# Kernel optimization log

Hardware: AMD Instinct MI355X
Metric: run time of the kernel (lower is better)

## Reference

```python
import jax, jax.numpy as jnp
import numpy as np

B, N, D = 8, 64, 512          # batch, latent tokens, token dim
C, H, W, P = 256, 128, 128, 36  # img feat channels/HW, sampling points
PG = 128                       # parameter-generator inner dim (0.25*D)
HEADS = 8                      # D // 64
TOT = C * C + P * P            # adaptive mixing param count per token


def _ln(x, g, b):
    m = x.mean(-1, keepdims=True)
    v = x.var(-1, keepdims=True)
    return (x - m) / jnp.sqrt(v + 1e-5) * g + b


def _gelu(x):
    return jax.nn.gelu(x, approximate=False)


def _grid_sample(img, grid):
    # img: (B,C,H,W); grid: (B,N,P,2) in [-1,1]; bilinear, border pad, align_corners=False
    Bi, Ci, Hi, Wi = img.shape
    x = ((grid[..., 0] + 1.0) * Wi - 1.0) * 0.5
    y = ((grid[..., 1] + 1.0) * Hi - 1.0) * 0.5
    x0 = jnp.floor(x)
    y0 = jnp.floor(y)
    wx = x - x0
    wy = y - y0
    x0i = jnp.clip(x0.astype(jnp.int32), 0, Wi - 1)
    x1i = jnp.clip(x0.astype(jnp.int32) + 1, 0, Wi - 1)
    y0i = jnp.clip(y0.astype(jnp.int32), 0, Hi - 1)
    y1i = jnp.clip(y0.astype(jnp.int32) + 1, 0, Hi - 1)
    imgt = img.transpose(0, 2, 3, 1)  # (B,H,W,C)
    bidx = jnp.arange(Bi)[:, None, None]
    v00 = imgt[bidx, y0i, x0i]  # (B,N,P,C)
    v01 = imgt[bidx, y0i, x1i]
    v10 = imgt[bidx, y1i, x0i]
    v11 = imgt[bidx, y1i, x1i]
    wx = wx[..., None]
    wy = wy[..., None]
    return (v00 * (1 - wx) * (1 - wy) + v01 * wx * (1 - wy)
            + v10 * (1 - wx) * wy + v11 * wx * wy)


def setup_inputs() -> dict:
    key = jax.random.key(0)
    ks = jax.random.split(key, 16)
    rn = lambda k, s, sc: jax.random.normal(k, s, jnp.float32) * sc
    tl = jax.random.uniform(ks[0], (B, N, 2), jnp.float32) * 0.5
    wh = 0.2 + jax.random.uniform(ks[1], (B, N, 2), jnp.float32) * 0.4
    return dict(
        token_embed=rn(ks[2], (B, N, D), 1.0),
        token_roi=jnp.concatenate([tl, tl + wh], axis=-1),
        img_feat=rn(ks[3], (B, C, H, W), 1.0),
        ln_off_g=jnp.ones(D), ln_off_b=jnp.zeros(D),
        w_off=rn(ks[4], (D, P * 2), D ** -0.5),
        roi_offset_bias=rn(ks[5], (P * 2,), 1.0),
        ln_pg_g=jnp.ones(D), ln_pg_b=jnp.zeros(D),
        w_pg1=rn(ks[6], (D, PG), D ** -0.5), b_pg1=jnp.zeros(PG),
        w_pg2=rn(ks[7], (PG, TOT), 0.02 * PG ** -0.5),
        b_pg2=rn(ks[8], (TOT,), 0.02),
        m_beta=jnp.zeros(C), s_beta=jnp.zeros(P),
        w_out=rn(ks[9], (P * C, D), (P * C) ** -0.5), b_out=jnp.zeros(D),
        ln1_g=jnp.ones(D), ln1_b=jnp.zeros(D),
        w_qkv=rn(ks[10], (D, 3 * D), D ** -0.5), b_qkv=jnp.zeros(3 * D),
        w_proj=rn(ks[11], (D, D), D ** -0.5), b_proj=jnp.zeros(D),
        ln2_g=jnp.ones(D), ln2_b=jnp.zeros(D),
        w_fc1=rn(ks[12], (D, 4 * D), D ** -0.5), b_fc1=jnp.zeros(4 * D),
        w_fc2=rn(ks[13], (4 * D, D), (4 * D) ** -0.5), b_fc2=jnp.zeros(D),
    )


def reference(token_embed, token_roi, img_feat,
              ln_off_g, ln_off_b, w_off, roi_offset_bias,
              ln_pg_g, ln_pg_b, w_pg1, b_pg1, w_pg2, b_pg2,
              m_beta, s_beta, w_out, b_out,
              ln1_g, ln1_b, w_qkv, b_qkv, w_proj, b_proj,
              ln2_g, ln2_b, w_fc1, b_fc1, w_fc2, b_fc2):
    Bq, Nq, Dm = token_embed.shape
    # --- OP.SAMPLING_M: offsets -> absolute points (n_heads=1) ---
    off = _ln(token_embed, ln_off_g, ln_off_b) @ w_off + roi_offset_bias  # (B,N,2P)
    off = off.reshape(Bq, Nq, 1, P, 2)
    mu = off.mean(-2, keepdims=True)
    sd = jnp.std(off, axis=-2, keepdims=True, ddof=1) + 1e-5  # unbiased, as torch.std
    off = (off - mu) / (3.0 * sd)
    xy = (token_roi[..., 2:] + token_roi[..., :2]) * 0.5
    wh = token_roi[..., 2:] - token_roi[..., :2]
    pts = xy[:, :, None, None, :] + off * wh[:, :, None, None, :]  # (B,N,1,P,2)
    grid = pts.reshape(Bq, Nq, P, 2) * 2.0 - 1.0
    sampled = _grid_sample(img_feat, grid)  # (B,N,P,C)
    # --- adaptive mixing (AdaMixer): per-token generated channel/spatial weights ---
    q = _ln(token_embed, ln_pg_g, ln_pg_b)
    params = (q @ w_pg1 + b_pg1) @ w_pg2 + b_pg2  # (B,N,TOT)
    cm = params[..., :C * C].reshape(Bq, Nq, C, C)
    sm = params[..., C * C:].reshape(Bq, Nq, P, P)
    h = _gelu(jnp.einsum('bnpc,bncd->bnpd', sampled, cm) + m_beta)
    h = _gelu(jnp.einsum('bnqp,bnpd->bnqd', sm, h) + s_beta[:, None])
    token_embed = token_embed + (h.reshape(Bq, Nq, P * C) @ w_out + b_out)
    # --- OP.ATTN ---
    x = _ln(token_embed, ln1_g, ln1_b)
    hd = Dm // HEADS
    qkv = (x @ w_qkv + b_qkv).reshape(Bq, Nq, 3, HEADS, hd)
    qh, kh, vh = qkv[:, :, 0], qkv[:, :, 1], qkv[:, :, 2]
    att = jax.nn.softmax(jnp.einsum('bqhd,bkhd->bhqk', qh, kh) * hd ** -0.5, axis=-1)
    o = jnp.einsum('bhqk,bkhd->bqhd', att, vh).reshape(Bq, Nq, Dm)
    token_embed = token_embed + (o @ w_proj + b_proj)
    # --- OP.MLP ---
    x = _ln(token_embed, ln2_g, ln2_b)
    token_embed = token_embed + (_gelu(x @ w_fc1 + b_fc1) @ w_fc2 + b_fc2)
    return token_embed
```

## Files before the change

### kernel.cpp

```cpp
#include <hip/hip_runtime.h>
#include <hip/hip_bf16.h>

typedef __hip_bfloat16 bf16;
typedef __attribute__((ext_vector_type(8))) short short8;
typedef __attribute__((ext_vector_type(4))) short s16x4;
typedef __attribute__((ext_vector_type(4))) float f32x4;

#define NTOK 512
#define TOTC 66832
#define CM_SZ 65536

__device__ __forceinline__ float b2f(bf16 x) { return __bfloat162float(x); }
__device__ __forceinline__ bf16 f2b(float x) { return __float2bfloat16(x); }
__device__ __forceinline__ float gelu_f(float x) {
  return 0.5f * x * (1.0f + erff(x * 0.7071067811865476f));
}
__device__ __forceinline__ f32x4 mfma16(short8 a, short8 b, f32x4 c) {
  return __builtin_amdgcn_mfma_f32_16x16x32_bf16(a, b, c, 0, 0, 0);
}

__global__ __launch_bounds__(256) void k_head(
    const float* __restrict__ te, const float* __restrict__ roi,
    const float* __restrict__ g_off, const float* __restrict__ b_off,
    const float* __restrict__ w_off, const float* __restrict__ off_bias,
    const float* __restrict__ g_pg, const float* __restrict__ b_pg,
    const float* __restrict__ w_pg1, const float* __restrict__ b_pg1,
    bf16* __restrict__ t_out, int* __restrict__ meta_i, float* __restrict__ meta_w,
    const float* __restrict__ img, bf16* __restrict__ imgT,
    const float* __restrict__ w0, bf16* __restrict__ o0,
    const float* __restrict__ w1, bf16* __restrict__ o1,
    const float* __restrict__ w2, bf16* __restrict__ o2,
    const float* __restrict__ w3, bf16* __restrict__ o3,
    const float* __restrict__ w4, bf16* __restrict__ o4) {
  __shared__ __align__(16) char smem_raw[16896];
  int blk = blockIdx.x;
  int t = threadIdx.x;
  if (blk < 512) {
    int tok = blk;
    int lane = t & 63, w = t >> 6;
    float* xo = (float*)smem_raw;
    float* xq = xo + 512;
    float* offb = xq + 512;
    float* red = offb + 72;
    float* wsum = red + 4;
    size_t base = (size_t)tok * 512;
    float a0 = te[base + t];
    float a1 = te[base + t + 256];
    float s = a0 + a1;
#pragma unroll
    for (int o = 32; o; o >>= 1) s += __shfl_xor(s, o);
    if (lane == 0) wsum[w] = s;
    __syncthreads();
    float mean = (wsum[0] + wsum[1] + wsum[2] + wsum[3]) * (1.0f / 512.0f);
    float d0 = a0 - mean, d1 = a1 - mean;
    float ss = d0 * d0 + d1 * d1;
#pragma unroll
    for (int o = 32; o; o >>= 1) ss += __shfl_xor(ss, o);
    __syncthreads();
    if (lane == 0) wsum[w] = ss;
    __syncthreads();
    float var = (wsum[0] + wsum[1] + wsum[2] + wsum[3]) * (1.0f / 512.0f);
    float rstd = rsqrtf(var + 1e-5f);
    xo[t] = d0 * rstd * g_off[t] + b_off[t];
    xo[t + 256] = d1 * rstd * g_off[t + 256] + b_off[t + 256];
    xq[t] = d0 * rstd * g_pg[t] + b_pg[t];
    xq[t + 256] = d1 * rstd * g_pg[t + 256] + b_pg[t + 256];
    __syncthreads();
    if (t < 128) {
      float acc = b_pg1[t];
      for (int d = 0; d < 512; ++d) acc = fmaf(xq[d], w_pg1[d * 128 + t], acc);
      t_out[(size_t)tok * 128 + t] = f2b(acc);
    } else if (t < 200) {
      int j = t - 128;
      float acc = off_bias[j];
      for (int d = 0; d < 512; ++d) acc = fmaf(xo[d], w_off[d * 72 + j], acc);
      offb[j] = acc;
    }
    __syncthreads();
    if (t < 2) {
      float mu = 0.f;
      for (int p = 0; p < 36; ++p) mu += offb[p * 2 + t];
      mu *= (1.0f / 36.0f);
      float s2 = 0.f;
      for (int p = 0; p < 36; ++p) { float dd = offb[p * 2 + t] - mu; s2 += dd * dd; }
      float sd = sqrtf(s2 * (1.0f / 35.0f)) + 1e-5f;
      red[t] = mu;
      red[2 + t] = 1.0f / (3.0f * sd);
    }
    __syncthreads();
    if (t < 36) {
      int p = t;
      float r0 = roi[tok * 4 + 0], r1 = roi[tok * 4 + 1];
      float r2 = roi[tok * 4 + 2], r3 = roi[tok * 4 + 3];
      float cx = (r0 + r2) * 0.5f, cy = (r1 + r3) * 0.5f;
      float bw = r2 - r0, bh = r3 - r1;
      float ox = (offb[p * 2 + 0] - red[0]) * red[2];
      float oy = (offb[p * 2 + 1] - red[1]) * red[3];
      float fx = (cx + ox * bw) * 128.0f - 0.5f;
      float fy = (cy + oy * bh) * 128.0f - 0.5f;
      float x0f = floorf(fx), y0f = floorf(fy);
      float wx = fx - x0f, wy = fy - y0f;
      int x0 = min(max((int)x0f, 0), 127);
      int x1 = min(max((int)x0f + 1, 0), 127);
      int y0 = min(max((int)y0f, 0), 127);
      int y1 = min(max((int)y0f + 1, 0), 127);
      int ibase = (tok >> 6) * 16384;
      int mi = (tok * 36 + p) * 4;
      meta_i[mi + 0] = (ibase + y0 * 128 + x0) * 256;
      meta_i[mi + 1] = (ibase + y0 * 128 + x1) * 256;
      meta_i[mi + 2] = (ibase + y1 * 128 + x0) * 256;
      meta_i[mi + 3] = (ibase + y1 * 128 + x1) * 256;
      meta_w[mi + 0] = (1.f - wx) * (1.f - wy);
      meta_w[mi + 1] = wx * (1.f - wy);
      meta_w[mi + 2] = (1.f - wx) * wy;
      meta_w[mi + 3] = wx * wy;
    }
  } else if (blk < 4608) {
    int bb = blk - 512;
    int b = bb >> 9;
    int hw0 = (bb & 511) * 32;
    bf16 (*tile2)[264] = (bf16(*)[264])smem_raw;
    int hw = t & 31, c0 = t >> 5;
#pragma unroll 8
    for (int i = 0; i < 32; ++i) {
      int c = c0 + 8 * i;
      tile2[hw][c] = f2b(img[((size_t)(b * 256 + c) << 14) + hw0 + hw]);
    }
    __syncthreads();
    int c8 = (t & 31) * 8, hwl = t >> 5;
#pragma unroll
    for (int p = 0; p < 4; ++p) {
      int h2 = hwl + 8 * p;
      *(short8*)&imgT[(((size_t)b << 14) + hw0 + h2) * 256 + c8] =
          *(const short8*)&tile2[h2][c8];
    }
  } else {
    int b = blk - 4608;
    const float* W;
    bf16* O;
    int K, N, loc;
    if (b < 4608) { W = w0; O = o0; K = 9216; N = 512; loc = b; }
    else if (b < 5376) { W = w1; O = o1; K = 512; N = 1536; loc = b - 4608; }
    else if (b < 5632) { W = w2; O = o2; K = 512; N = 512; loc = b - 5376; }
    else if (b < 6656) { W = w3; O = o3; K = 512; N = 2048; loc = b - 5632; }
    else { W = w4; O = o4; K = 2048; N = 512; loc = b - 6656; }
    int ntn = N >> 5;
    int nb = loc % ntn, kb = loc / ntn;
    int n0 = nb * 32, k0 = kb * 32;
    float (*tl)[33] = (float(*)[33])smem_raw;
    int r = t >> 5, c = t & 31;
#pragma unroll
    for (int i = 0; i < 4; ++i)
      tl[r + 8 * i][c] = W[(size_t)(k0 + r + 8 * i) * N + n0 + c];
    __syncthreads();
    int n_l = t >> 3, k4 = (t & 7) * 4;
    bf16 tmp[4];
#pragma unroll
    for (int j = 0; j < 4; ++j) tmp[j] = f2b(tl[k4 + j][n_l]);
    *(s16x4*)&O[(size_t)(n0 + n_l) * K + k0 + k4] = *(const s16x4*)tmp;
  }
}

__global__ __launch_bounds__(256) void k_samp_pg2(
    const bf16* __restrict__ tb16, const float* __restrict__ w2,
    const float* __restrict__ b2, bf16* __restrict__ pchunk,
    const bf16* __restrict__ imgT, const int* __restrict__ meta_i,
    const float* __restrict__ meta_w, bf16* __restrict__ S) {
  __shared__ bf16 BsT[64][136];
  int blk = blockIdx.x;
  int t = threadIdx.x;
  if (blk < 2090) {
    int n0 = (blk % 1045) * 64;
    int row0 = (blk / 1045) * 256;
    int lane = t & 63, w = t >> 6;
    int quad = lane >> 4, l16 = lane & 15;
    {
      int nl = (t & 15) * 4, kk = t >> 4;
#pragma unroll
      for (int pass = 0; pass < 8; ++pass) {
        int k = kk + pass * 16;
        int n = n0 + nl;
        int nc = (n + 3 < TOTC) ? n : (TOTC - 4);
        const float4 v = *(const float4*)(w2 + (size_t)k * TOTC + nc);
        BsT[nl + 0][k] = f2b(v.x);
        BsT[nl + 1][k] = f2b(v.y);
        BsT[nl + 2][k] = f2b(v.z);
        BsT[nl + 3][k] = f2b(v.w);
      }
    }
    __syncthreads();
    f32x4 acc[4][4];
#pragma unroll
    for (int i = 0; i < 4; ++i)
#pragma unroll
      for (int j = 0; j < 4; ++j) acc[i][j] = (f32x4){0.f, 0.f, 0.f, 0.f};
    const bf16* Abase = tb16 + ((size_t)(row0 + w * 64 + l16)) * 128 + quad * 8;
#pragma unroll
    for (int ks = 0; ks < 4; ++ks) {
      short8 af[4], bff[4];
#pragma unroll
      for (int mt = 0; mt < 4; ++mt)
        af[mt] = *(const short8*)(Abase + mt * 16 * 128 + ks * 32);
#pragma unroll
      for (int nt = 0; nt < 4; ++nt)
        bff[nt] = *(const short8*)(&BsT[nt * 16 + l16][ks * 32 + quad * 8]);
#pragma unroll
      for (int mt = 0; mt < 4; ++mt)
#pragma unroll
        for (int nt = 0; nt < 4; ++nt)
          acc[mt][nt] = mfma16(af[mt], bff[nt], acc[mt][nt]);
    }
    float bias_r[4];
#pragma unroll
    for (int nt = 0; nt < 4; ++nt) {
      int col = n0 + nt * 16 + l16;
      bias_r[nt] = (col < TOTC) ? b2[col] : 0.f;
    }
    bf16* stg = &BsT[0][0];
#pragma unroll
    for (int mt = 0; mt < 4; ++mt) {
      __syncthreads();
#pragma unroll
      for (int nt = 0; nt < 4; ++nt)
#pragma unroll
        for (int r = 0; r < 4; ++r)
          stg[(w * 16 + quad * 4 + r) * 72 + nt * 16 + l16] =
              f2b(acc[mt][nt][r] + bias_r[nt]);
      __syncthreads();
#pragma unroll
      for (int pass = 0; pass < 2; ++pass) {
        int t2 = t + pass * 256;
        int row_l = t2 >> 3;
        int wi = row_l >> 4, rr = row_l & 15;
        int c8 = (t2 & 7) * 8;
        int col = n0 + c8;
        if (col < TOTC) {
          int grow = row0 + wi * 64 + mt * 16 + rr;
          *(short8*)&pchunk[(size_t)grow * TOTC + col] =
              *(const short8*)&stg[(wi * 16 + rr) * 72 + c8];
        }
      }
    }
  } else {
    int tok = blk - 2090;
#pragma unroll 6
    for (int p = 0; p < 36; ++p) {
      int mi = (tok * 36 + p) * 4;
      int o00 = meta_i[mi + 0], o01 = meta_i[mi + 1], o10 = meta_i[mi + 2], o11 = meta_i[mi + 3];
      float w00 = meta_w[mi + 0], w01 = meta_w[mi + 1], w10 = meta_w[mi + 2], w11 = meta_w[mi + 3];
      float v = w00 * b2f(imgT[o00 + t]) + w01 * b2f(imgT[o01 + t]) +
                w10 * b2f(imgT[o10 + t]) + w11 * b2f(imgT[o11 + t]);
      S[((size_t)tok * 36 + p) * 256 + t] = f2b(v);
    }
  }
}

__global__ __launch_bounds__(256) void k_mix3(const bf16* __restrict__ pchunk,
                                              const bf16* __restrict__ S,
                                              const float* __restrict__ m_beta,
                                              const float* __restrict__ s_beta,
                                              bf16* __restrict__ h2) {
  int tok = blockIdx.x, dh = blockIdx.y * 128;
  int t = threadIdx.x, lane = t & 63, w = t >> 6;
  int quad = lane >> 4, l16 = lane & 15;
  __shared__ bf16 h1T[128][72];
  __shared__ bf16 smS[48][72];
  __shared__ short cmw[4][32][40];
  for (int i = t; i < 1728; i += 256) ((unsigned*)smS)[i] = 0u;
  __syncthreads();
  const bf16* sm = pchunk + (size_t)tok * TOTC + CM_SZ;
  for (int i = t; i < 1296; i += 256) {
    int q = i / 36, p = i - q * 36;
    smS[q][p] = sm[i];
  }
  f32x4 acc[3][2];
#pragma unroll
  for (int i = 0; i < 3; ++i)
#pragma unroll
    for (int j = 0; j < 2; ++j) acc[i][j] = (f32x4){0.f, 0.f, 0.f, 0.f};
  const bf16* Sg = S + (size_t)tok * 9216;
  const bf16* Cg = pchunk + (size_t)tok * TOTC;
  int dw = w * 32;
  int c_l = lane & 31;
  int dtop = (lane >> 5) * 16;
  const bf16* src0 = Cg + (size_t)c_l * 256 + dh + dw + dtop;
  short8 v0 = *(const short8*)src0;
  short8 v1 = *(const short8*)(src0 + 8);
#pragma unroll
  for (int kc = 0; kc < 256; kc += 32) {
#pragma unroll
    for (int j = 0; j < 8; ++j) cmw[w][dtop + j][c_l] = v0[j];
#pragma unroll
    for (int j = 0; j < 8; ++j) cmw[w][dtop + 8 + j][c_l] = v1[j];
    short8 a[3];
#pragma unroll
    for (int mt = 0; mt < 3; ++mt)
      a[mt] = *(const short8*)(Sg + (size_t)(mt * 16 + l16) * 256 + kc + quad * 8);
    short8 v0n, v1n;
    if (kc < 224) {
      const bf16* srcn = Cg + (size_t)(kc + 32 + c_l) * 256 + dh + dw + dtop;
      v0n = *(const short8*)srcn;
      v1n = *(const short8*)(srcn + 8);
    }
    asm volatile("" ::: "memory");
    short8 bfr[2];
#pragma unroll
    for (int nt = 0; nt < 2; ++nt)
      bfr[nt] = *(const short8*)&cmw[w][nt * 16 + l16][quad * 8];
#pragma unroll
    for (int mt = 0; mt < 3; ++mt)
#pragma unroll
      for (int nt = 0; nt < 2; ++nt)
        acc[mt][nt] = mfma16(a[mt], bfr[nt], acc[mt][nt]);
    asm volatile("" ::: "memory");
    v0 = v0n;
    v1 = v1n;
  }
#pragma unroll
  for (int nt = 0; nt < 2; ++nt) {
    int dl = dw + nt * 16 + l16;
    float mb = m_beta[dh + dl];
#pragma unroll
    for (int mt = 0; mt < 3; ++mt)
#pragma unroll
      for (int r = 0; r < 4; ++r) {
        int p = mt * 16 + quad * 4 + r;
        if (p < 36) h1T[dl][p] = f2b(gelu_f(acc[mt][nt][r] + mb));
      }
  }
  for (int i = t; i < 128 * 28; i += 256) {
    int d = i / 28, p = 36 + i % 28;
    h1T[d][p] = (bf16)0.f;
  }
  __syncthreads();
  f32x4 acc2[3][2];
#pragma unroll
  for (int i = 0; i < 3; ++i)
#pragma unroll
    for (int j = 0; j < 2; ++j) acc2[i][j] = (f32x4){0.f, 0.f, 0.f, 0.f};
#pragma unroll
  for (int ks = 0; ks < 2; ++ks) {
    short8 a2[3], b2v[2];
#pragma unroll
    for (int mt = 0; mt < 3; ++mt)
      a2[mt] = *(const short8*)&smS[mt * 16 + l16][ks * 32 + quad * 8];
#pragma unroll
    for (int nt = 0; nt < 2; ++nt)
      b2v[nt] = *(const short8*)&h1T[dw + nt * 16 + l16][ks * 32 + quad * 8];
#pragma unroll
    for (int mt = 0; mt < 3; ++mt)
#pragma unroll
      for (int nt = 0; nt < 2; ++nt)
        acc2[mt][nt] = mfma16(a2[mt], b2v[nt], acc2[mt][nt]);
  }
  bf16* h2p = h2 + (size_t)tok * 9216 + dh;
#pragma unroll
  for (int mt = 0; mt < 3; ++mt)
#pragma unroll
    for (int r = 0; r < 4; ++r) {
      int q = mt * 16 + quad * 4 + r;
      if (q >= 36) continue;
      float sb = s_beta[q];
#pragma unroll
      for (int nt = 0; nt < 2; ++nt)
        h2p[q * 256 + dw + nt * 16 + l16] = f2b(gelu_f(acc2[mt][nt][r] + sb));
    }
}

__global__ __launch_bounds__(256) void k_gemm_bt(const bf16* __restrict__ A,
                                                 const bf16* __restrict__ BT,
                                                 float* __restrict__ part,
                                                 int M, int N, int K) {
  int nb = blockIdx.x, mb = blockIdx.y, ks = blockIdx.z;
  int kchunk = K / gridDim.z;
  int k0 = ks * kchunk;
  __shared__ bf16 As[64][72], Bs[64][72];
  int t = threadIdx.x, lane = t & 63, w = t >> 6;
  int quad = lane >> 4, l16 = lane & 15;
  int wm = (w >> 1) * 32, wn = (w & 1) * 32;
  int r = t >> 2, kk = (t & 3) * 16;
  f32x4 acc[2][2];
#pragma unroll
  for (int i = 0; i < 2; ++i)
#pragma unroll
    for (int j = 0; j < 2; ++j) acc[i][j] = (f32x4){0.f, 0.f, 0.f, 0.f};
  for (int kt = 0; kt < kchunk; kt += 64) {
    __syncthreads();
    const bf16* ga = A + (size_t)(mb * 64 + r) * K + k0 + kt + kk;
    *(short8*)&As[r][kk] = *(const short8*)ga;
    *(short8*)&As[r][kk + 8] = *(const short8*)(ga + 8);
    const bf16* gb = BT + (size_t)(nb * 64 + r) * K + k0 + kt + kk;
    *(short8*)&Bs[r][kk] = *(const short8*)gb;
    *(short8*)&Bs[r][kk + 8] = *(const short8*)(gb + 8);
    __syncthreads();
#pragma unroll
    for (int kss = 0; kss < 2; ++kss) {
      short8 af[2], bff[2];
#pragma unroll
      for (int mt = 0; mt < 2; ++mt)
        af[mt] = *(const short8*)&As[wm + mt * 16 + l16][kss * 32 + quad * 8];
#pragma unroll
      for (int nt = 0; nt < 2; ++nt)
        bff[nt] = *(const short8*)&Bs[wn + nt * 16 + l16][kss * 32 + quad * 8];
#pragma unroll
      for (int mt = 0; mt < 2; ++mt)
#pragma unroll
        for (int nt = 0; nt < 2; ++nt)
          acc[mt][nt] = mfma16(af[mt], bff[nt], acc[mt][nt]);
    }
  }
#pragma unroll
  for (int mt = 0; mt < 2; ++mt)
#pragma unroll
    for (int rr = 0; rr < 4; ++rr) {
      int m = mb * 64 + wm + mt * 16 + quad * 4 + rr;
#pragma unroll
      for (int nt = 0; nt < 2; ++nt) {
        int n = nb * 64 + wn + nt * 16 + l16;
        part[(size_t)ks * M * N + (size_t)m * N + n] = acc[mt][nt][rr];
      }
    }
}

__global__ __launch_bounds__(256) void k_gemm_ep(const bf16* __restrict__ A,
                                                 const bf16* __restrict__ BT,
                                                 const float* __restrict__ bias,
                                                 int M, int N, int K, int do_gelu,
                                                 float* __restrict__ outf,
                                                 bf16* __restrict__ outh) {
  int nb = blockIdx.x, mb = blockIdx.y;
  __shared__ bf16 As[64][72], Bs[64][72];
  int t = threadIdx.x, lane = t & 63, w = t >> 6;
  int quad = lane >> 4, l16 = lane & 15;
  int wm = (w >> 1) * 32, wn = (w & 1) * 32;
  int r = t >> 2, kk = (t & 3) * 16;
  f32x4 acc[2][2];
#pragma unroll
  for (int i = 0; i < 2; ++i)
#pragma unroll
    for (int j = 0; j < 2; ++j) acc[i][j] = (f32x4){0.f, 0.f, 0.f, 0.f};
  for (int kt = 0; kt < K; kt += 64) {
    __syncthreads();
    const bf16* ga = A + (size_t)(mb * 64 + r) * K + kt + kk;
    *(short8*)&As[r][kk] = *(const short8*)ga;
    *(short8*)&As[r][kk + 8] = *(const short8*)(ga + 8);
    const bf16* gb = BT + (size_t)(nb * 64 + r) * K + kt + kk;
    *(short8*)&Bs[r][kk] = *(const short8*)gb;
    *(short8*)&Bs[r][kk + 8] = *(const short8*)(gb + 8);
    __syncthreads();
#pragma unroll
    for (int kss = 0; kss < 2; ++kss) {
      short8 af[2], bff[2];
#pragma unroll
      for (int mt = 0; mt < 2; ++mt)
        af[mt] = *(const short8*)&As[wm + mt * 16 + l16][kss * 32 + quad * 8];
#pragma unroll
      for (int nt = 0; nt < 2; ++nt)
        bff[nt] = *(const short8*)&Bs[wn + nt * 16 + l16][kss * 32 + quad * 8];
#pragma unroll
      for (int mt = 0; mt < 2; ++mt)
#pragma unroll
        for (int nt = 0; nt < 2; ++nt)
          acc[mt][nt] = mfma16(af[mt], bff[nt], acc[mt][nt]);
    }
  }
#pragma unroll
  for (int mt = 0; mt < 2; ++mt)
#pragma unroll
    for (int rr = 0; rr < 4; ++rr) {
      int m = mb * 64 + wm + mt * 16 + quad * 4 + rr;
#pragma unroll
      for (int nt = 0; nt < 2; ++nt) {
        int n = nb * 64 + wn + nt * 16 + l16;
        float a = acc[mt][nt][rr] + bias[n];
        if (do_gelu) a = gelu_f(a);
        if (outf) outf[(size_t)m * N + n] = a;
        else outh[(size_t)m * N + n] = f2b(a);
      }
    }
}

__global__ __launch_bounds__(256) void k_epi(const float* __restrict__ part, int S_,
                                             int MN, int N, const float* __restrict__ bias,
                                             const float* __restrict__ resf, int do_gelu,
                                             float* __restrict__ outf, bf16* __restrict__ outh) {
  int idx = blockIdx.x * 256 + threadIdx.x;
  if (idx >= MN) return;
  int n = idx % N;
  float a = 0.f;
  for (int s = 0; s < S_; ++s) a += part[(size_t)s * MN + idx];
  a += bias[n];
  if (resf) a += resf[idx];
  if (do_gelu) a = gelu_f(a);
  if (outf) outf[idx] = a;
  if (outh) outh[idx] = f2b(a);
}

__global__ __launch_bounds__(256) void k_epi_ln(const float* __restrict__ part, int S_,
                                                const float* __restrict__ bias,
                                                const float* __restrict__ res,
                                                const float* __restrict__ g,
                                                const float* __restrict__ bvec,
                                                float* __restrict__ xout,
                                                bf16* __restrict__ lnout) {
  int tok = blockIdx.x, t = threadIdx.x, lane = t & 63, w = t >> 6;
  __shared__ float wsum[4];
  size_t base = (size_t)tok * 512;
  float a0 = bias[t] + res[base + t];
  float a1 = bias[t + 256] + res[base + t + 256];
  for (int sp = 0; sp < S_; ++sp) {
    const float* p = part + (size_t)sp * 262144 + base;
    a0 += p[t];
    a1 += p[t + 256];
  }
  xout[base + t] = a0;
  xout[base + t + 256] = a1;
  float s = a0 + a1;
#pragma unroll
  for (int o = 32; o; o >>= 1) s += __shfl_xor(s, o);
  if (lane == 0) wsum[w] = s;
  __syncthreads();
  float mean = (wsum[0] + wsum[1] + wsum[2] + wsum[3]) * (1.0f / 512.0f);
  float d0 = a0 - mean, d1 = a1 - mean;
  float ss = d0 * d0 + d1 * d1;
#pragma unroll
  for (int o = 32; o; o >>= 1) ss += __shfl_xor(ss, o);
  __syncthreads();
  if (lane == 0) wsum[w] = ss;
  __syncthreads();
  float var = (wsum[0] + wsum[1] + wsum[2] + wsum[3]) * (1.0f / 512.0f);
  float rstd = rsqrtf(var + 1e-5f);
  lnout[base + t] = f2b(d0 * rstd * g[t] + bvec[t]);
  lnout[base + t + 256] = f2b(d1 * rstd * g[t + 256] + bvec[t + 256]);
}

__global__ __launch_bounds__(256) void k_attn(const float* __restrict__ qkvf,
                                              bf16* __restrict__ obuf) {
  int b = blockIdx.x >> 3, h = blockIdx.x & 7;
  int q0 = blockIdx.y * 16;
  __shared__ float kT[64][65];
  __shared__ float vT[64][65];
  __shared__ float att[16][65];
  int t = threadIdx.x, lane = t & 63, w = t >> 6;
#pragma unroll
  for (int i = 0; i < 16; ++i) {
    int idx = t + i * 256;
    int j = idx >> 6, d = idx & 63;
    size_t tb = (size_t)(b * 64 + j) * 1536 + h * 64 + d;
    kT[j][d] = qkvf[tb + 512];
    vT[j][d] = qkvf[tb + 1024];
  }
  __syncthreads();
#pragma unroll
  for (int m = 0; m < 4; ++m) {
    int il = w * 4 + m;
    int i = q0 + il;
    const float* qrow = &qkvf[(size_t)(b * 64 + i) * 1536 + h * 64];
    float s = 0.f;
    for (int d = 0; d < 64; ++d) s = fmaf(qrow[d], kT[lane][d], s);
    s *= 0.125f;
    float mx = s;
#pragma unroll
    for (int o = 32; o; o >>= 1) mx = fmaxf(mx, __shfl_xor(mx, o));
    float e = expf(s - mx);
    float sum = e;
#pragma unroll
    for (int o = 32; o; o >>= 1) sum += __shfl_xor(sum, o);
    att[il][lane] = e / sum;
  }
  __syncthreads();
#pragma unroll
  for (int m = 0; m < 4; ++m) {
    int il = w * 4 + m;
    int i = q0 + il;
    float o = 0.f;
    for (int j = 0; j < 64; ++j) o = fmaf(att[il][j], vT[j][lane], o);
    obuf[(size_t)(b * 64 + i) * 512 + h * 64 + lane] = f2b(o);
  }
}

extern "C" void kernel_launch(void* const* d_in, const int* in_sizes, int n_in,
                              void* d_out, int out_size, void* d_ws, size_t ws_size,
                              hipStream_t stream) {
  const float* te = (const float*)d_in[0];
  const float* roi = (const float*)d_in[1];
  const float* img = (const float*)d_in[2];
  const float* ln_off_g = (const float*)d_in[3];
  const float* ln_off_b = (const float*)d_in[4];
  const float* w_off = (const float*)d_in[5];
  const float* off_bias = (const float*)d_in[6];
  const float* ln_pg_g = (const float*)d_in[7];
  const float* ln_pg_b = (const float*)d_in[8];
  const float* w_pg1 = (const float*)d_in[9];
  const float* b_pg1 = (const float*)d_in[10];
  const float* w_pg2 = (const float*)d_in[11];
  const float* b_pg2 = (const float*)d_in[12];
  const float* m_beta = (const float*)d_in[13];
  const float* s_beta = (const float*)d_in[14];
  const float* w_out = (const float*)d_in[15];
  const float* b_out = (const float*)d_in[16];
  const float* ln1_g = (const float*)d_in[17];
  const float* ln1_b = (const float*)d_in[18];
  const float* w_qkv = (const float*)d_in[19];
  const float* b_qkv = (const float*)d_in[20];
  const float* w_proj = (const float*)d_in[21];
  const float* b_proj = (const float*)d_in[22];
  const float* ln2_g = (const float*)d_in[23];
  const float* ln2_b = (const float*)d_in[24];
  const float* w_fc1 = (const float*)d_in[25];
  const float* b_fc1 = (const float*)d_in[26];
  const float* w_fc2 = (const float*)d_in[27];
  const float* b_fc2 = (const float*)d_in[28];

  char* ws = (char*)d_ws;
  bf16* imgT = (bf16*)ws;
  char* ov = ws;
  bf16* h2 = (bf16*)ov; ov += 9437184;
  float* part = (float*)ov; ov += 8388608;
  float* x1 = (float*)ov; ov += 1048576;
  float* xa = (float*)ov; ov += 1048576;
  float* qkvf = (float*)ov; ov += 3145728;
  bf16* ln1buf = (bf16*)ov; ov += 524288;
  bf16* ln2buf = (bf16*)ov; ov += 524288;
  bf16* obuf = (bf16*)ov; ov += 524288;
  bf16* hfc = (bf16*)ov; ov += 2097152;
  char* tail = ws + 67108864;
  bf16* Sbuf = (bf16*)tail; tail += 9437184;
  bf16* tb16 = (bf16*)tail; tail += 131072;
  int* meta_i = (int*)tail; tail += 294912;
  float* meta_w = (float*)tail; tail += 294912;
  bf16* pchunk = (bf16*)tail; tail += (size_t)NTOK * TOTC * 2;
  bf16* w_outT = (bf16*)tail; tail += 9437184;
  bf16* w_qkvT = (bf16*)tail; tail += 1572864;
  bf16* w_projT = (bf16*)tail; tail += 524288;
  bf16* w_fc1T = (bf16*)tail; tail += 2097152;
  bf16* w_fc2T = (bf16*)tail; tail += 2097152;
  (void)ws_size;

  k_head<<<12288, 256, 0, stream>>>(te, roi, ln_off_g, ln_off_b, w_off, off_bias,
                                    ln_pg_g, ln_pg_b, w_pg1, b_pg1, tb16, meta_i, meta_w,
                                    img, imgT,
                                    w_out, w_outT, w_qkv, w_qkvT, w_proj, w_projT,
                                    w_fc1, w_fc1T, w_fc2, w_fc2T);
  k_samp_pg2<<<2602, 256, 0, stream>>>(tb16, w_pg2, b_pg2, pchunk,
                                       imgT, meta_i, meta_w, Sbuf);
  k_mix3<<<dim3(512, 2), 256, 0, stream>>>(pchunk, Sbuf, m_beta, s_beta, h2);

  k_gemm_bt<<<dim3(8, 8, 8), 256, 0, stream>>>(h2, w_outT, part, 512, 512, 9216);
  k_epi_ln<<<512, 256, 0, stream>>>(part, 8, b_out, te, ln1_g, ln1_b, x1, ln1buf);

  k_gemm_ep<<<dim3(24, 8), 256, 0, stream>>>(ln1buf, w_qkvT, b_qkv, 512, 1536, 512, 0,
                                             qkvf, nullptr);
  k_attn<<<dim3(64, 4), 256, 0, stream>>>(qkvf, obuf);
  k_gemm_bt<<<dim3(8, 8, 4), 256, 0, stream>>>(obuf, w_projT, part, 512, 512, 512);
  k_epi_ln<<<512, 256, 0, stream>>>(part, 4, b_proj, x1, ln2_g, ln2_b, xa, ln2buf);

  k_gemm_ep<<<dim3(32, 8), 256, 0, stream>>>(ln2buf, w_fc1T, b_fc1, 512, 2048, 512, 1,
                                             nullptr, hfc);
  k_gemm_bt<<<dim3(8, 8, 4), 256, 0, stream>>>(hfc, w_fc2T, part, 512, 512, 2048);
  k_epi<<<1024, 256, 0, stream>>>(part, 4, 512 * 512, 512, b_fc2, xa, 0, (float*)d_out, nullptr);
}
```

Baseline: 481.1 us.

## Vectorize image transpose, reuse pg2 weight tile across rows, fuse fc2 epilogue

The image NCHW→NHWC bf16 transpose now reads float4 per thread and uses a 64-pixel tile with an XOR swizzle to avoid LDS bank conflicts. The parameter-generator GEMM block now covers both 256-row halves with one loaded weight tile, so the large w_pg2 matrix is read and converted once instead of twice. The final fc2 GEMM uses the bias/residual epilogue GEMM directly, removing split-K partials and the separate reduction kernel. Risks: fewer blocks in the pg2 stage and the no-split-K fc2 with K=2048 on only 64 blocks may lose parallelism.

```diff
diff --git a/kernel.cpp b/kernel.cpp
--- a/kernel.cpp
+++ b/kernel.cpp
@@ -32,7 +32,7 @@
     const float* __restrict__ w2, bf16* __restrict__ o2,
     const float* __restrict__ w3, bf16* __restrict__ o3,
     const float* __restrict__ w4, bf16* __restrict__ o4) {
-  __shared__ __align__(16) char smem_raw[16896];
+  __shared__ __align__(16) char smem_raw[36864];
   int blk = blockIdx.x;
   int t = threadIdx.x;
   if (blk < 512) {
@@ -115,27 +115,39 @@
       meta_w[mi + 2] = (1.f - wx) * wy;
       meta_w[mi + 3] = wx * wy;
     }
-  } else if (blk < 4608) {
+  } else if (blk < 2560) {
     int bb = blk - 512;
-    int b = bb >> 9;
-    int hw0 = (bb & 511) * 32;
-    bf16 (*tile2)[264] = (bf16(*)[264])smem_raw;
-    int hw = t & 31, c0 = t >> 5;
-#pragma unroll 8
-    for (int i = 0; i < 32; ++i) {
-      int c = c0 + 8 * i;
-      tile2[hw][c] = f2b(img[((size_t)(b * 256 + c) << 14) + hw0 + hw]);
-    }
-    __syncthreads();
-    int c8 = (t & 31) * 8, hwl = t >> 5;
-#pragma unroll
-    for (int p = 0; p < 4; ++p) {
-      int h2 = hwl + 8 * p;
-      *(short8*)&imgT[(((size_t)b << 14) + hw0 + h2) * 256 + c8] =
-          *(const short8*)&tile2[h2][c8];
+    int b = bb >> 8;
+    int hw0 = (bb & 255) * 64;
+    bf16 (*tl)[72] = (bf16(*)[72])smem_raw;
+    int hw_l = (t & 15) * 4;
+#pragma unroll
+    for (int pass = 0; pass < 16; ++pass) {
+      int c = (t >> 4) + 16 * pass;
+      const float4 v = *(const float4*)&img[((size_t)(b * 256 + c) << 14) + hw0 + hw_l];
+      float vv[4] = {v.x, v.y, v.z, v.w};
+      int mask = ((c >> 3) & 31) << 1;
+      int base = hw_l ^ (mask & 60);
+      int swp = mask & 2;
+      bf16 o[4];
+#pragma unroll
+      for (int k = 0; k < 4; ++k) o[k] = f2b(vv[k ^ swp]);
+      *(s16x4*)&tl[c][base] = *(const s16x4*)o;
+    }
+    __syncthreads();
+    int c8 = (t & 31) * 8;
+    int hwb = t >> 5;
+    int rmask = ((c8 >> 3) & 31) << 1;
+#pragma unroll
+    for (int pass = 0; pass < 8; ++pass) {
+      int hw = hwb + 8 * pass;
+      bf16 tmp[8];
+#pragma unroll
+      for (int j = 0; j < 8; ++j) tmp[j] = tl[c8 + j][hw ^ rmask];
+      *(short8*)&imgT[((size_t)(b << 14) + hw0 + hw) * 256 + c8] = *(const short8*)tmp;
     }
   } else {
-    int b = blk - 4608;
+    int b = blk - 2560;
     const float* W;
     bf16* O;
     int K, N, loc;
@@ -147,16 +159,16 @@
     int ntn = N >> 5;
     int nb = loc % ntn, kb = loc / ntn;
     int n0 = nb * 32, k0 = kb * 32;
-    float (*tl)[33] = (float(*)[33])smem_raw;
+    float (*tw)[33] = (float(*)[33])smem_raw;
     int r = t >> 5, c = t & 31;
 #pragma unroll
     for (int i = 0; i < 4; ++i)
-      tl[r + 8 * i][c] = W[(size_t)(k0 + r + 8 * i) * N + n0 + c];
+      tw[r + 8 * i][c] = W[(size_t)(k0 + r + 8 * i) * N + n0 + c];
     __syncthreads();
     int n_l = t >> 3, k4 = (t & 7) * 4;
     bf16 tmp[4];
 #pragma unroll
-    for (int j = 0; j < 4; ++j) tmp[j] = f2b(tl[k4 + j][n_l]);
+    for (int j = 0; j < 4; ++j) tmp[j] = f2b(tw[k4 + j][n_l]);
     *(s16x4*)&O[(size_t)(n0 + n_l) * K + k0 + k4] = *(const s16x4*)tmp;
   }
 }
@@ -167,11 +179,11 @@
     const bf16* __restrict__ imgT, const int* __restrict__ meta_i,
     const float* __restrict__ meta_w, bf16* __restrict__ S) {
   __shared__ bf16 BsT[64][136];
+  __shared__ bf16 stg[64][72];
   int blk = blockIdx.x;
   int t = threadIdx.x;
-  if (blk < 2090) {
-    int n0 = (blk % 1045) * 64;
-    int row0 = (blk / 1045) * 256;
+  if (blk < 1045) {
+    int n0 = blk * 64;
     int lane = t & 63, w = t >> 6;
     int quad = lane >> 4, l16 = lane & 15;
     {
@@ -189,60 +201,63 @@
       }
     }
     __syncthreads();
-    f32x4 acc[4][4];
-#pragma unroll
-    for (int i = 0; i < 4; ++i)
-#pragma unroll
-      for (int j = 0; j < 4; ++j) acc[i][j] = (f32x4){0.f, 0.f, 0.f, 0.f};
-    const bf16* Abase = tb16 + ((size_t)(row0 + w * 64 + l16)) * 128 + quad * 8;
-#pragma unroll
-    for (int ks = 0; ks < 4; ++ks) {
-      short8 af[4], bff[4];
-#pragma unroll
-      for (int mt = 0; mt < 4; ++mt)
-        af[mt] = *(const short8*)(Abase + mt * 16 * 128 + ks * 32);
-#pragma unroll
-      for (int nt = 0; nt < 4; ++nt)
-        bff[nt] = *(const short8*)(&BsT[nt * 16 + l16][ks * 32 + quad * 8]);
-#pragma unroll
-      for (int mt = 0; mt < 4; ++mt)
-#pragma unroll
-        for (int nt = 0; nt < 4; ++nt)
-          acc[mt][nt] = mfma16(af[mt], bff[nt], acc[mt][nt]);
-    }
     float bias_r[4];
 #pragma unroll
     for (int nt = 0; nt < 4; ++nt) {
       int col = n0 + nt * 16 + l16;
       bias_r[nt] = (col < TOTC) ? b2[col] : 0.f;
     }
-    bf16* stg = &BsT[0][0];
-#pragma unroll
-    for (int mt = 0; mt < 4; ++mt) {
-      __syncthreads();
-#pragma unroll
-      for (int nt = 0; nt < 4; ++nt)
-#pragma unroll
-        for (int r = 0; r < 4; ++r)
-          stg[(w * 16 + quad * 4 + r) * 72 + nt * 16 + l16] =
-              f2b(acc[mt][nt][r] + bias_r[nt]);
-      __syncthreads();
-#pragma unroll
-      for (int pass = 0; pass < 2; ++pass) {
-        int t2 = t + pass * 256;
-        int row_l = t2 >> 3;
-        int wi = row_l >> 4, rr = row_l & 15;
-        int c8 = (t2 & 7) * 8;
-        int col = n0 + c8;
-        if (col < TOTC) {
-          int grow = row0 + wi * 64 + mt * 16 + rr;
-          *(short8*)&pchunk[(size_t)grow * TOTC + col] =
-              *(const short8*)&stg[(wi * 16 + rr) * 72 + c8];
+    for (int half = 0; half < 2; ++half) {
+      int row0 = half * 256;
+      f32x4 acc[4][4];
+#pragma unroll
+      for (int i = 0; i < 4; ++i)
+#pragma unroll
+        for (int j = 0; j < 4; ++j) acc[i][j] = (f32x4){0.f, 0.f, 0.f, 0.f};
+      const bf16* Abase = tb16 + ((size_t)(row0 + w * 64 + l16)) * 128 + quad * 8;
+#pragma unroll
+      for (int ks = 0; ks < 4; ++ks) {
+        short8 af[4], bff[4];
+#pragma unroll
+        for (int mt = 0; mt < 4; ++mt)
+          af[mt] = *(const short8*)(Abase + mt * 16 * 128 + ks * 32);
+#pragma unroll
+        for (int nt = 0; nt < 4; ++nt)
+          bff[nt] = *(const short8*)(&BsT[nt * 16 + l16][ks * 32 + quad * 8]);
+#pragma unroll
+        for (int mt = 0; mt < 4; ++mt)
+#pragma unroll
+          for (int nt = 0; nt < 4; ++nt)
+            acc[mt][nt] = mfma16(af[mt], bff[nt], acc[mt][nt]);
+      }
+#pragma unroll
+      for (int mt = 0; mt < 4; ++mt) {
+        __syncthreads();
+#pragma unroll
+        for (int nt = 0; nt < 4; ++nt)
+#pragma unroll
+          for (int r = 0; r < 4; ++r)
+            stg[w * 16 + quad * 4 + r][nt * 16 + l16] =
+                f2b(acc[mt][nt][r] + bias_r[nt]);
+        __syncthreads();
+#pragma unroll
+        for (int pass = 0; pass < 2; ++pass) {
+          int t2 = t + pass * 256;
+          int row_l = t2 >> 3;
+          int wi = row_l >> 4, rr = row_l & 15;
+          int c8 = (t2 & 7) * 8;
+          int col = n0 + c8;
+          if (col < TOTC) {
+            int grow = row0 + wi * 64 + mt * 16 + rr;
+            *(short8*)&pchunk[(size_t)grow * TOTC + col] =
+                *(const short8*)&stg[wi * 16 + rr][c8];
+          }
         }
       }
+      __syncthreads();
     }
   } else {
-    int tok = blk - 2090;
+    int tok = blk - 1045;
 #pragma unroll 6
     for (int p = 0; p < 36; ++p) {
       int mi = (tok * 36 + p) * 4;
@@ -426,6 +441,7 @@
                                                  const bf16* __restrict__ BT,
                                                  const float* __restrict__ bias,
                                                  int M, int N, int K, int do_gelu,
+                                                 const float* __restrict__ resf,
                                                  float* __restrict__ outf,
                                                  bf16* __restrict__ outh) {
   int nb = blockIdx.x, mb = blockIdx.y;
@@ -473,27 +489,12 @@
       for (int nt = 0; nt < 2; ++nt) {
         int n = nb * 64 + wn + nt * 16 + l16;
         float a = acc[mt][nt][rr] + bias[n];
+        if (resf) a += resf[(size_t)m * N + n];
         if (do_gelu) a = gelu_f(a);
         if (outf) outf[(size_t)m * N + n] = a;
         else outh[(size_t)m * N + n] = f2b(a);
       }
     }
-}
-
-__global__ __launch_bounds__(256) void k_epi(const float* __restrict__ part, int S_,
-                                             int MN, int N, const float* __restrict__ bias,
-                                             const float* __restrict__ resf, int do_gelu,
-                                             float* __restrict__ outf, bf16* __restrict__ outh) {
-  int idx = blockIdx.x * 256 + threadIdx.x;
-  if (idx >= MN) return;
-  int n = idx % N;
-  float a = 0.f;
-  for (int s = 0; s < S_; ++s) a += part[(size_t)s * MN + idx];
-  a += bias[n];
-  if (resf) a += resf[idx];
-  if (do_gelu) a = gelu_f(a);
-  if (outf) outf[idx] = a;
-  if (outh) outh[idx] = f2b(a);
 }
 
 __global__ __launch_bounds__(256) void k_epi_ln(const float* __restrict__ part, int S_,
@@ -637,12 +638,12 @@
   bf16* w_fc2T = (bf16*)tail; tail += 2097152;
   (void)ws_size;
 
-  k_head<<<12288, 256, 0, stream>>>(te, roi, ln_off_g, ln_off_b, w_off, off_bias,
+  k_head<<<10240, 256, 0, stream>>>(te, roi, ln_off_g, ln_off_b, w_off, off_bias,
                                     ln_pg_g, ln_pg_b, w_pg1, b_pg1, tb16, meta_i, meta_w,
                                     img, imgT,
                                     w_out, w_outT, w_qkv, w_qkvT, w_proj, w_projT,
                                     w_fc1, w_fc1T, w_fc2, w_fc2T);
-  k_samp_pg2<<<2602, 256, 0, stream>>>(tb16, w_pg2, b_pg2, pchunk,
+  k_samp_pg2<<<1557, 256, 0, stream>>>(tb16, w_pg2, b_pg2, pchunk,
                                        imgT, meta_i, meta_w, Sbuf);
   k_mix3<<<dim3(512, 2), 256, 0, stream>>>(pchunk, Sbuf, m_beta, s_beta, h2);
 
@@ -650,13 +651,13 @@
   k_epi_ln<<<512, 256, 0, stream>>>(part, 8, b_out, te, ln1_g, ln1_b, x1, ln1buf);
 
   k_gemm_ep<<<dim3(24, 8), 256, 0, stream>>>(ln1buf, w_qkvT, b_qkv, 512, 1536, 512, 0,
-                                             qkvf, nullptr);
+                                             nullptr, qkvf, nullptr);
   k_attn<<<dim3(64, 4), 256, 0, stream>>>(qkvf, obuf);
   k_gemm_bt<<<dim3(8, 8, 4), 256, 0, stream>>>(obuf, w_projT, part, 512, 512, 512);
   k_epi_ln<<<512, 256, 0, stream>>>(part, 4, b_proj, x1, ln2_g, ln2_b, xa, ln2buf);
 
   k_gemm_ep<<<dim3(32, 8), 256, 0, stream>>>(ln2buf, w_fc1T, b_fc1, 512, 2048, 512, 1,
-                                             nullptr, hfc);
-  k_gemm_bt<<<dim3(8, 8, 4), 256, 0, stream>>>(hfc, w_fc2T, part, 512, 512, 2048);
-  k_epi<<<1024, 256, 0, stream>>>(part, 4, 512 * 512, 512, b_fc2, xa, 0, (float*)d_out, nullptr);
-}
+                                             nullptr, nullptr, hfc);
+  k_gemm_ep<<<dim3(8, 8), 256, 0, stream>>>(hfc, w_fc2T, b_fc2, 512, 512, 2048, 0,
+                                            xa, (float*)d_out, nullptr);
+}
```

Measured after the change: 487.4 us. No clear change (+1.3%).
